# Kernel optimization log

Hardware: AMD Instinct MI355X
Metric: run time of the kernel (lower is better)

The kernel has to match this reference:

```python
import jax, jax.numpy as jnp
import numpy as np

B, C, F, H, W = 2, 512, 8, 32, 32


def setup_inputs() -> dict:
    key = jax.random.key(0)
    ks = jax.random.split(key, 10)
    s = 0.02
    return {
        "x": jax.random.normal(ks[0], (B, C, F, H, W), jnp.float32),
        "gamma": jnp.ones((C, 1, 1, 1), jnp.float32),
        "wq": jax.random.normal(ks[1], (C, C), jnp.float32) * s,
        "bq": jnp.zeros((C,), jnp.float32),
        "wk": jax.random.normal(ks[2], (C, C), jnp.float32) * s,
        "bk": jnp.zeros((C,), jnp.float32),
        "wv": jax.random.normal(ks[3], (C, C), jnp.float32) * s,
        "bv": jnp.zeros((C,), jnp.float32),
        "wo": jax.random.normal(ks[4], (C, C), jnp.float32) * s,
        "bo": jnp.zeros((C,), jnp.float32),
    }


def _rms_norm(x, gamma):
    # F.normalize(x, dim=1) * sqrt(C) * gamma  (channel-first, eps=1e-12)
    n = jnp.sqrt(jnp.sum(x * x, axis=1, keepdims=True))
    return x / jnp.maximum(n, 1e-12) * (x.shape[1] ** 0.5) * gamma


def _conv1x1(x, w, b):
    # 1x1x1 Conv3d == per-voxel linear over channels
    return jnp.einsum("oi,bifhw->bofhw", w, x) + b[None, :, None, None, None]


def reference(x, gamma, wq, bq, wk, bk, wv, bv, wo, bo):
    b, c, f, h, w = x.shape
    n_hw = h * w
    S = f * n_hw

    hn = _rms_norm(x, gamma)
    q = _conv1x1(hn, wq, bq).reshape(b, c, S).swapaxes(1, 2)  # [b, S, c]
    k = _conv1x1(hn, wk, bk).reshape(b, c, S).swapaxes(1, 2)
    v = _conv1x1(hn, wv, bv).reshape(b, c, S).swapaxes(1, 2)

    # block-causal mask: query attends to all tokens in frames <= its own frame
    frame_id = jnp.arange(S) // n_hw
    allow = frame_id[:, None] >= frame_id[None, :]  # [S, S] bool

    scores = jnp.einsum("bsc,btc->bst", q, k) / jnp.sqrt(jnp.asarray(c, x.dtype))
    scores = jnp.where(allow[None], scores, -jnp.inf)
    p = jax.nn.softmax(scores, axis=-1)
    o = jnp.einsum("bst,btc->bsc", p, v)  # [b, S, c]

    o = o.swapaxes(1, 2).reshape(b, c, f, h, w)
    return x + _conv1x1(o, wo, bo)
```

## Files before the change

### kernel.cpp

```cpp
#include <hip/hip_runtime.h>
#include <hip/hip_bf16.h>
#include <math.h>

typedef __bf16 bf16;
typedef __bf16 bf16x8 __attribute__((ext_vector_type(8)));
typedef float f32x4 __attribute__((ext_vector_type(4)));
typedef long longx2 __attribute__((ext_vector_type(2)));

#define C_DIM 512
#define S_DIM 8192

__device__ __forceinline__ void async_ld16(const void* g, void* l) {
    __builtin_amdgcn_global_load_lds(
        (const __attribute__((address_space(1))) unsigned int*)g,
        (__attribute__((address_space(3))) unsigned int*)l, 16, 0, 0);
}

__device__ __forceinline__ unsigned char to_fp8(float v) {
    return (unsigned char)(__builtin_amdgcn_cvt_pk_fp8_f32(v, v, 0, false) & 0xFF);
}

__global__ void detect_kernel(const unsigned short* __restrict__ xu, int* __restrict__ flag) {
    int j = threadIdx.x;
    for (int i = 16 + j; i < 320; i += 64) flag[i] = 0;
    unsigned e = (xu[2 * j] >> 7) & 0xFF;
    unsigned long long m = __ballot(e >= 90 && e <= 140);
    if (j == 0) *flag = (__popcll(m) >= 48) ? 1 : 0;
}

__global__ __launch_bounds__(256) void convert_kernel(const void* __restrict__ s0,
                                                      const void* __restrict__ s1,
                                                      const void* __restrict__ s2,
                                                      const void* __restrict__ s3,
                                                      bf16* __restrict__ dst,
                                                      const int* __restrict__ flag) {
    int y = blockIdx.y;
    const void* srcs[4] = {s0, s1, s2, s3};
    const void* src = srcs[y];
    int i = blockIdx.x * 256 + threadIdx.x;
    bf16* d = dst + (size_t)y * 262144;
    if (*flag) {
        volatile const bf16* s = (volatile const bf16*)src;
        d[i] = s[i];
    } else {
        volatile const float* s = (volatile const float*)src;
        d[i] = (bf16)s[i];
    }
}

__global__ __launch_bounds__(256) void rms_kernel(const void* __restrict__ x,
                                                  float* __restrict__ r,
                                                  const int* __restrict__ flag) {
    __shared__ float red[4][64];
    int b  = blockIdx.x >> 7;
    int s0 = (blockIdx.x & 127) * 64;
    int sl = threadIdx.x & 63;
    int cq = threadIdx.x >> 6;
    float acc = 0.f;
    if (*flag) {
        const bf16* xp = (const bf16*)x + ((size_t)b * C_DIM + cq * 128) * S_DIM + s0 + sl;
        for (int c = 0; c < 128; ++c) { float v = (float)xp[(size_t)c * S_DIM]; acc += v * v; }
    } else {
        const float* xp = (const float*)x + ((size_t)b * C_DIM + cq * 128) * S_DIM + s0 + sl;
        for (int c = 0; c < 128; ++c) { float v = xp[(size_t)c * S_DIM]; acc += v * v; }
    }
    red[cq][sl] = acc;
    __syncthreads();
    if (cq == 0) {
        float t = red[0][sl] + red[1][sl] + red[2][sl] + red[3][sl];
        r[b * S_DIM + s0 + sl] = 22.627416997969522f / fmaxf(sqrtf(t), 1e-12f);
    }
}

__global__ __launch_bounds__(256) void hn_kernel(const void* __restrict__ x,
                                                 const void* __restrict__ gamma,
                                                 const float* __restrict__ r,
                                                 bf16* __restrict__ hn,
                                                 const int* __restrict__ flag) {
    __shared__ float tile[64][65];
    int f  = *flag;
    int b  = blockIdx.z;
    int c0 = blockIdx.y * 64;
    int s0 = blockIdx.x * 64;
    int col = threadIdx.x & 63;
    int row = threadIdx.x >> 6;
    if (f) {
        const bf16* xp = (const bf16*)x + ((size_t)b * C_DIM + c0) * S_DIM + s0;
        for (int i = 0; i < 16; ++i)
            tile[row + i * 4][col] = (float)xp[(size_t)(row + i * 4) * S_DIM + col];
    } else {
        const float* xp = (const float*)x + ((size_t)b * C_DIM + c0) * S_DIM + s0;
        for (int i = 0; i < 16; ++i)
            tile[row + i * 4][col] = xp[(size_t)(row + i * 4) * S_DIM + col];
    }
    __syncthreads();
    float g;
    if (f) g = (float)((const bf16*)gamma)[c0 + col];
    else   g = ((const float*)gamma)[c0 + col];
    bf16* hp = hn + ((size_t)b * S_DIM + s0) * C_DIM + c0;
    for (int i = 0; i < 16; ++i) {
        int s_l = row + i * 4;
        float rv = r[b * S_DIM + s0 + s_l];
        hp[(size_t)s_l * C_DIM + col] = (bf16)(tile[col][s_l] * rv * g);
    }
}

__global__ __launch_bounds__(256, 2) void gemm_qkv_kernel(const bf16* __restrict__ A,
                                                          const bf16* __restrict__ Wq,
                                                          const bf16* __restrict__ Wk,
                                                          const bf16* __restrict__ Wv,
                                                          const void* __restrict__ bq,
                                                          const void* __restrict__ bk,
                                                          const void* __restrict__ bv,
                                                          unsigned char* __restrict__ oq,
                                                          unsigned char* __restrict__ ok,
                                                          unsigned char* __restrict__ ov,
                                                          const int* __restrict__ flag) {
    __shared__ bf16 As[128 * 40];
    __shared__ bf16 Bqs[128 * 40];
    __shared__ bf16 Bks[128 * 40];
    __shared__ bf16 Bvs[128 * 40];
    int f  = *flag;
    int m0 = blockIdx.x * 128;
    int n0 = blockIdx.y * 128;
    int tid  = threadIdx.x;
    int lane = tid & 63;
    int wave = tid >> 6;
    int wm = (wave & 1) * 64;
    int wn = (wave >> 1) * 64;
    int l15  = lane & 15;
    int quad = lane >> 4;

    f32x4 aq[4][4] = {}, ak[4][4] = {}, av[4][4] = {};
    for (int k0 = 0; k0 < C_DIM; k0 += 32) {
        __syncthreads();
        for (int u = tid; u < 512; u += 256) {
            int rr = u >> 2;
            int cc = (u & 3) * 8;
            *(bf16x8*)&As[rr * 40 + cc]  = *(const bf16x8*)&A [(size_t)(m0 + rr) * C_DIM + k0 + cc];
            *(bf16x8*)&Bqs[rr * 40 + cc] = *(const bf16x8*)&Wq[(size_t)(n0 + rr) * C_DIM + k0 + cc];
            *(bf16x8*)&Bks[rr * 40 + cc] = *(const bf16x8*)&Wk[(size_t)(n0 + rr) * C_DIM + k0 + cc];
            *(bf16x8*)&Bvs[rr * 40 + cc] = *(const bf16x8*)&Wv[(size_t)(n0 + rr) * C_DIM + k0 + cc];
        }
        __syncthreads();
        bf16x8 af[4];
#pragma unroll
        for (int i = 0; i < 4; ++i)
            af[i] = *(bf16x8*)&As[(wm + i * 16 + l15) * 40 + quad * 8];
#pragma unroll
        for (int j = 0; j < 4; ++j) {
            int boff = (wn + j * 16 + l15) * 40 + quad * 8;
            bf16x8 b0 = *(bf16x8*)&Bqs[boff];
#pragma unroll
            for (int i = 0; i < 4; ++i)
                aq[i][j] = __builtin_amdgcn_mfma_f32_16x16x32_bf16(af[i], b0, aq[i][j], 0, 0, 0);
            bf16x8 b1 = *(bf16x8*)&Bks[boff];
#pragma unroll
            for (int i = 0; i < 4; ++i)
                ak[i][j] = __builtin_amdgcn_mfma_f32_16x16x32_bf16(af[i], b1, ak[i][j], 0, 0, 0);
            bf16x8 b2 = *(bf16x8*)&Bvs[boff];
#pragma unroll
            for (int i = 0; i < 4; ++i)
                av[i][j] = __builtin_amdgcn_mfma_f32_16x16x32_bf16(af[i], b2, av[i][j], 0, 0, 0);
        }
    }
#pragma unroll
    for (int i = 0; i < 4; ++i)
#pragma unroll
        for (int j = 0; j < 4; ++j) {
            int n = n0 + wn + j * 16 + l15;
            float bvq = f ? (float)((const bf16*)bq)[n] : ((const float*)bq)[n];
            float bvk = f ? (float)((const bf16*)bk)[n] : ((const float*)bk)[n];
            float bvv = f ? (float)((const bf16*)bv)[n] : ((const float*)bv)[n];
#pragma unroll
            for (int rg = 0; rg < 4; ++rg) {
                int m = m0 + wm + i * 16 + quad * 4 + rg;
                oq[(size_t)m * C_DIM + n] = to_fp8(aq[i][j][rg] + bvq);
                size_t ik = (size_t)(m >> 5) * 16384 +
                            (((size_t)(n >> 6) * 4 + ((n >> 3) & 3)) * 32 + (m & 31)) * 16 +
                            ((n >> 5) & 1) * 8 + (n & 7);
                ok[ik] = to_fp8(ak[i][j][rg] + bvk);
                size_t iv = (size_t)(m >> 5) * 16384 + ((size_t)(m >> 3) & 3) * 4096 +
                            (((size_t)(n >> 5) * 16 + (n & 15)) * 2 + ((n >> 4) & 1)) * 8 + (m & 7);
                ov[iv] = to_fp8(av[i][j][rg] + bvv);
            }
        }
}

__global__ __launch_bounds__(256, 2) void gemm_kernel(const bf16* __restrict__ A,
                                                      const bf16* __restrict__ W,
                                                      const void* __restrict__ bias,
                                                      const void* __restrict__ resid,
                                                      void* __restrict__ out,
                                                      const int* __restrict__ flag) {
    __shared__ bf16 As[128 * 40];
    __shared__ bf16 Bs[128 * 40];
    int f  = *flag;
    int m0 = blockIdx.x * 128;
    int n0 = blockIdx.y * 128;
    int tid  = threadIdx.x;
    int lane = tid & 63;
    int wave = tid >> 6;
    int wm = (wave & 1) * 64;
    int wn = (wave >> 1) * 64;
    int l15  = lane & 15;
    int quad = lane >> 4;

    f32x4 acc[4][4] = {};
    for (int k0 = 0; k0 < C_DIM; k0 += 32) {
        __syncthreads();
        for (int u = tid; u < 512; u += 256) {
            int rrow = u >> 2;
            int cc = (u & 3) * 8;
            *(bf16x8*)&As[rrow * 40 + cc] =
                *(const bf16x8*)&A[(size_t)(m0 + rrow) * C_DIM + k0 + cc];
            *(bf16x8*)&Bs[rrow * 40 + cc] =
                *(const bf16x8*)&W[(size_t)(n0 + rrow) * C_DIM + k0 + cc];
        }
        __syncthreads();
        bf16x8 af[4], bfr[4];
#pragma unroll
        for (int i = 0; i < 4; ++i)
            af[i] = *(bf16x8*)&As[(wm + i * 16 + l15) * 40 + quad * 8];
#pragma unroll
        for (int j = 0; j < 4; ++j)
            bfr[j] = *(bf16x8*)&Bs[(wn + j * 16 + l15) * 40 + quad * 8];
#pragma unroll
        for (int i = 0; i < 4; ++i)
#pragma unroll
            for (int j = 0; j < 4; ++j)
                acc[i][j] = __builtin_amdgcn_mfma_f32_16x16x32_bf16(af[i], bfr[j], acc[i][j], 0, 0, 0);
    }
    if (f) {
        bf16* op = (bf16*)out;
        const bf16* rp = (const bf16*)resid;
#pragma unroll
        for (int i = 0; i < 4; ++i)
#pragma unroll
            for (int j = 0; j < 4; ++j)
#pragma unroll
                for (int rg = 0; rg < 4; ++rg) {
                    int m = m0 + wm + i * 16 + quad * 4 + rg;
                    int n = n0 + wn + j * 16 + l15;
                    float bv = (float)((const bf16*)bias)[n];
                    int b = m >> 13, s = m & 8191;
                    size_t idx = ((size_t)b * C_DIM + n) * S_DIM + s;
                    op[idx] = (bf16)(acc[i][j][rg] + bv + (float)rp[idx]);
                }
    } else {
        float* op = (float*)out;
        const float* rp = (const float*)resid;
#pragma unroll
        for (int i = 0; i < 4; ++i)
#pragma unroll
            for (int j = 0; j < 4; ++j)
#pragma unroll
                for (int rg = 0; rg < 4; ++rg) {
                    int m = m0 + wm + i * 16 + quad * 4 + rg;
                    int n = n0 + wn + j * 16 + l15;
                    float bv = ((const float*)bias)[n];
                    int b = m >> 13, s = m & 8191;
                    size_t idx = ((size_t)b * C_DIM + n) * S_DIM + s;
                    op[idx] = acc[i][j][rg] + bv + rp[idx];
                }
    }
}

__global__ __launch_bounds__(256, 2) void attn_split_kernel(const unsigned char* __restrict__ q,
                                                            const unsigned char* __restrict__ k,
                                                            const unsigned char* __restrict__ vt,
                                                            bf16* __restrict__ part,
                                                            float* __restrict__ lsum,
                                                            int* __restrict__ counter,
                                                            int* __restrict__ cnt,
                                                            int* __restrict__ slist) {
    __shared__ unsigned char Ks[2][16384];
    __shared__ unsigned char Vs[2][16384];
    __shared__ unsigned char Ps[4][16 * 40];
    __shared__ int slot_sh;
    int tid  = threadIdx.x;
    int lane = tid & 63;
    int wave = tid >> 6;
    int l15  = lane & 15;
    int quad = lane >> 4;

    int g0 = blockIdx.x * 72;
    int b_ = (g0 >= 18432) ? 1 : 0;
    int r  = g0 - b_ * 18432;
    int f_ = 0;
    while (r >= 256 * (f_ + 1) * (f_ + 2)) ++f_;
    int L   = 32 * (f_ + 1);
    int rr  = r - 256 * f_ * (f_ + 1);
    int tif = rr / L;
    int cw  = rr - tif * L;

    long qf[16];
    {
        int qbase = (f_ * 16 + tif) * 64 + wave * 16;
        const unsigned char* qp = q + (size_t)(b_ * S_DIM + qbase + l15) * C_DIM;
#pragma unroll
        for (int ks = 0; ks < 16; ++ks)
            qf[ks] = *(const long*)&qp[ks * 32 + quad * 8];
    }

    f32x4 oacc[32] = {};
    float l_i[4] = {0.f, 0.f, 0.f, 0.f};
    const float scale = 0.044194173824159216f;

    {
        const unsigned char* ka = k  + ((size_t)(b_ * 256 + cw) << 14);
        const unsigned char* va = vt + ((size_t)(b_ * 256 + cw) << 14);
#pragma unroll
        for (int j = 0; j < 4; ++j) {
            int base = (j * 4 + wave) * 1024;
            async_ld16(ka + base + lane * 16, &Ks[0][base]);
            async_ld16(va + base + lane * 16, &Vs[0][base]);
        }
    }
    __syncthreads();

    for (int i = 0; i < 72; ++i) {
        int last = (i == 71);
        int nb = b_, nf = f_, nL = L, ntif = tif, ncw = cw + 1;
        int newtile = 0;
        if (ncw == L) {
            ncw = 0; newtile = 1; ntif = tif + 1;
            if (ntif == 16) {
                ntif = 0; nf = f_ + 1; nL = L + 32;
                if (nf == 8) { nf = 0; nL = 32; nb = b_ + 1; }
            }
        }
        if (last) { nb = b_; nf = f_; nL = L; ntif = tif; ncw = cw; newtile = 0; }

        {
            const unsigned char* ka = k  + ((size_t)(nb * 256 + ncw) << 14);
            const unsigned char* va = vt + ((size_t)(nb * 256 + ncw) << 14);
            unsigned char* kd = Ks[(i + 1) & 1];
            unsigned char* vd = Vs[(i + 1) & 1];
#pragma unroll
            for (int j = 0; j < 4; ++j) {
                int base = (j * 4 + wave) * 1024;
                async_ld16(ka + base + lane * 16, kd + base);
                async_ld16(va + base + lane * 16, vd + base);
            }
        }
        const unsigned char* kb = Ks[i & 1];
        const unsigned char* vb = Vs[i & 1];

        f32x4 st[2] = {};
#pragma unroll
        for (int nt = 0; nt < 2; ++nt) {
#pragma unroll
            for (int pp = 0; pp < 8; ++pp) {
                longx2 kf = *(const longx2*)&kb[(((pp * 4 + quad) * 32) + nt * 16 + l15) * 16];
                st[nt] = __builtin_amdgcn_mfma_f32_16x16x32_fp8_fp8(qf[2 * pp], kf[0], st[nt], 0, 0, 0);
                st[nt] = __builtin_amdgcn_mfma_f32_16x16x32_fp8_fp8(qf[2 * pp + 1], kf[1], st[nt], 0, 0, 0);
            }
        }
        float p0[4], p1[4];
#pragma unroll
        for (int rg = 0; rg < 4; ++rg) {
            p0[rg] = __expf(st[0][rg] * scale);
            p1[rg] = __expf(st[1][rg] * scale);
            l_i[rg] += p0[rg] + p1[rg];
        }
        unsigned char* pw = Ps[wave];
#pragma unroll
        for (int rg = 0; rg < 4; ++rg) {
            pw[(quad * 4 + rg) * 40 + l15] = to_fp8(p0[rg]);
            pw[(quad * 4 + rg) * 40 + 16 + l15] = to_fp8(p1[rg]);
        }
        long pf = *(const long*)&pw[l15 * 40 + quad * 8];
#pragma unroll
        for (int dnp = 0; dnp < 16; ++dnp) {
            longx2 vf = *(const longx2*)&vb[quad * 4096 + (dnp * 16 + l15) * 16];
            oacc[2 * dnp]     = __builtin_amdgcn_mfma_f32_16x16x32_fp8_fp8(pf, vf[0], oacc[2 * dnp], 0, 0, 0);
            oacc[2 * dnp + 1] = __builtin_amdgcn_mfma_f32_16x16x32_fp8_fp8(pf, vf[1], oacc[2 * dnp + 1], 0, 0, 0);
        }

        if (last || newtile) {
            int ord = b_ * 128 + f_ * 16 + tif;
            if (tid == 0) {
                int s = atomicAdd(counter, 1);
                int pos = atomicAdd(&cnt[ord], 1);
                slist[ord * 8 + pos] = s;
                slot_sh = s;
            }
            __syncthreads();
            int slot = slot_sh;
#pragma unroll
            for (int rg = 0; rg < 4; ++rg)
                for (int d = 1; d < 16; d <<= 1)
                    l_i[rg] += __shfl_xor(l_i[rg], d);
            float rinv[4];
#pragma unroll
            for (int rg = 0; rg < 4; ++rg) rinv[rg] = 1.f / l_i[rg];
            bf16* pp = part + ((size_t)slot * 64 + wave * 16) * C_DIM;
#pragma unroll
            for (int dn = 0; dn < 32; ++dn)
#pragma unroll
                for (int rg = 0; rg < 4; ++rg)
                    pp[(size_t)(quad * 4 + rg) * C_DIM + dn * 16 + l15] =
                        (bf16)(oacc[dn][rg] * rinv[rg]);
            if (l15 == 0) {
#pragma unroll
                for (int rg = 0; rg < 4; ++rg)
                    lsum[slot * 64 + wave * 16 + quad * 4 + rg] = l_i[rg];
            }
            if (!last) {
#pragma unroll
                for (int dn = 0; dn < 32; ++dn) oacc[dn] = (f32x4){0.f, 0.f, 0.f, 0.f};
#pragma unroll
                for (int rg = 0; rg < 4; ++rg) l_i[rg] = 0.f;
                int nqbase = (nf * 16 + ntif) * 64 + wave * 16;
                const unsigned char* qp = q + (size_t)(nb * S_DIM + nqbase + l15) * C_DIM;
#pragma unroll
                for (int ks = 0; ks < 16; ++ks)
                    qf[ks] = *(const long*)&qp[ks * 32 + quad * 8];
            }
        }
        b_ = nb; f_ = nf; L = nL; tif = ntif; cw = ncw;
        __syncthreads();
    }
}

__global__ __launch_bounds__(256, 2) void attn_kernel(const unsigned char* __restrict__ q,
                                                      const unsigned char* __restrict__ k,
                                                      const unsigned char* __restrict__ vt,
                                                      bf16* __restrict__ ob) {
    __shared__ unsigned char Ks[2][16384];
    __shared__ unsigned char Vs[2][16384];
    __shared__ unsigned char Ps[4][16 * 40];
    int id = blockIdx.x;
    int b = id >> 7;
    int t = id & 127;
    int q0 = t * 64;
    int kc1 = ((t >> 4) + 1) << 10;
    int tid  = threadIdx.x;
    int lane = tid & 63;
    int wave = tid >> 6;
    int l15  = lane & 15;
    int quad = lane >> 4;
    int qbase = q0 + wave * 16;
    int nchunks = kc1 >> 5;

    long qf[16];
    const unsigned char* qp = q + (size_t)(b * S_DIM + qbase + l15) * C_DIM;
#pragma unroll
    for (int ks = 0; ks < 16; ++ks)
        qf[ks] = *(const long*)&qp[ks * 32 + quad * 8];

    f32x4 oacc[32] = {};
    float l_i[4] = {0.f, 0.f, 0.f, 0.f};
    const float scale = 0.044194173824159216f;

    const unsigned char* kbase = k  + ((size_t)(b * 256) << 14);
    const unsigned char* vbase = vt + ((size_t)(b * 256) << 14);

#pragma unroll
    for (int j = 0; j < 4; ++j) {
        int base = (j * 4 + wave) * 1024;
        async_ld16(kbase + base + lane * 16, &Ks[0][base]);
        async_ld16(vbase + base + lane * 16, &Vs[0][base]);
    }
    __syncthreads();

    for (int p = 0; p < nchunks; ++p) {
        int pn = (p + 1 < nchunks) ? (p + 1) : p;
        const unsigned char* ksub = kbase + ((size_t)pn << 14);
        const unsigned char* vsub = vbase + ((size_t)pn << 14);
        unsigned char* kd = Ks[(p + 1) & 1];
        unsigned char* vd = Vs[(p + 1) & 1];
#pragma unroll
        for (int j = 0; j < 4; ++j) {
            int base = (j * 4 + wave) * 1024;
            async_ld16(ksub + base + lane * 16, kd + base);
            async_ld16(vsub + base + lane * 16, vd + base);
        }
        const unsigned char* kb = Ks[p & 1];
        const unsigned char* vb = Vs[p & 1];
        f32x4 st[2] = {};
#pragma unroll
        for (int nt = 0; nt < 2; ++nt) {
#pragma unroll
            for (int pp = 0; pp < 8; ++pp) {
                longx2 kf = *(const longx2*)&kb[(((pp * 4 + quad) * 32) + nt * 16 + l15) * 16];
                st[nt] = __builtin_amdgcn_mfma_f32_16x16x32_fp8_fp8(qf[2 * pp], kf[0], st[nt], 0, 0, 0);
                st[nt] = __builtin_amdgcn_mfma_f32_16x16x32_fp8_fp8(qf[2 * pp + 1], kf[1], st[nt], 0, 0, 0);
            }
        }
        float p0[4], p1[4];
#pragma unroll
        for (int rg = 0; rg < 4; ++rg) {
            p0[rg] = __expf(st[0][rg] * scale);
            p1[rg] = __expf(st[1][rg] * scale);
            l_i[rg] += p0[rg] + p1[rg];
        }
        unsigned char* pw = Ps[wave];
#pragma unroll
        for (int rg = 0; rg < 4; ++rg) {
            pw[(quad * 4 + rg) * 40 + l15] = to_fp8(p0[rg]);
            pw[(quad * 4 + rg) * 40 + 16 + l15] = to_fp8(p1[rg]);
        }
        long pf = *(const long*)&pw[l15 * 40 + quad * 8];
#pragma unroll
        for (int dnp = 0; dnp < 16; ++dnp) {
            longx2 vf = *(const longx2*)&vb[quad * 4096 + (dnp * 16 + l15) * 16];
            oacc[2 * dnp]     = __builtin_amdgcn_mfma_f32_16x16x32_fp8_fp8(pf, vf[0], oacc[2 * dnp], 0, 0, 0);
            oacc[2 * dnp + 1] = __builtin_amdgcn_mfma_f32_16x16x32_fp8_fp8(pf, vf[1], oacc[2 * dnp + 1], 0, 0, 0);
        }
        __syncthreads();
    }
#pragma unroll
    for (int rg = 0; rg < 4; ++rg)
        for (int d = 1; d < 16; d <<= 1)
            l_i[rg] += __shfl_xor(l_i[rg], d);
    float rinv[4];
#pragma unroll
    for (int rg = 0; rg < 4; ++rg) rinv[rg] = 1.f / l_i[rg];
    bf16* op = ob + (size_t)(b * S_DIM + qbase) * C_DIM;
#pragma unroll
    for (int dn = 0; dn < 32; ++dn)
#pragma unroll
        for (int rg = 0; rg < 4; ++rg)
            op[(size_t)(quad * 4 + rg) * C_DIM + dn * 16 + l15] =
                (bf16)(oacc[dn][rg] * rinv[rg]);
}

__global__ __launch_bounds__(256) void combine_kernel(const bf16* __restrict__ part,
                                                      const float* __restrict__ lsum,
                                                      bf16* __restrict__ ob,
                                                      const int* __restrict__ cnt,
                                                      const int* __restrict__ slist) {
    int id = blockIdx.x;
    int b  = id >> 7;
    int q0 = (id & 127) * 64;
    int U  = cnt[id];
    int qq = threadIdx.x >> 2;
    int cr = threadIdx.x & 3;
    int sl[8];
    float w[8];
    float D = 0.f;
    for (int u = 0; u < U; ++u) {
        sl[u] = slist[id * 8 + u];
        w[u] = lsum[sl[u] * 64 + qq];
        D += w[u];
    }
    float Dinv = 1.f / D;
    for (int u = 0; u < U; ++u) w[u] *= Dinv;
    bf16* op = ob + (size_t)(b * S_DIM + q0 + qq) * C_DIM + cr * 128;
    for (int ch = 0; ch < 16; ++ch) {
        float acc[8] = {};
        for (int u = 0; u < U; ++u) {
            bf16x8 pv = *(const bf16x8*)&part[((size_t)sl[u] * 64 + qq) * C_DIM + cr * 128 + ch * 8];
#pragma unroll
            for (int j = 0; j < 8; ++j) acc[j] += w[u] * (float)pv[j];
        }
        bf16x8 o8;
#pragma unroll
        for (int j = 0; j < 8; ++j) o8[j] = (bf16)acc[j];
        *(bf16x8*)&op[ch * 8] = o8;
    }
}

extern "C" void kernel_launch(void* const* d_in, const int* in_sizes, int n_in,
                              void* d_out, int out_size, void* d_ws, size_t ws_size,
                              hipStream_t stream) {
    const void* x     = d_in[0];
    const void* gamma = d_in[1];
    const void* wq    = d_in[2];
    const void* bq    = d_in[3];
    const void* wk    = d_in[4];
    const void* bk    = d_in[5];
    const void* wv    = d_in[6];
    const void* bv    = d_in[7];
    const void* wo    = d_in[8];
    const void* bo    = d_in[9];

    char* ws = (char*)d_ws;
    int*   flag    = (int*)ws;
    int*   counter = (int*)(ws + 64);
    int*   cntp    = (int*)(ws + 256);
    int*   slist   = (int*)(ws + 0x12000);
    float* r_buf   = (float*)(ws + 4096);
    bf16* wqb = (bf16*)(ws + 0x20000);
    bf16* wkb = (bf16*)(ws + 0xA0000);
    bf16* wvb = (bf16*)(ws + 0x120000);
    bf16* wob = (bf16*)(ws + 0x1A0000);
    float* lsum_buf = (float*)(ws + 0x240000);
    bf16* hn  = (bf16*)(ws + 0x400000);
    unsigned char* qb  = (unsigned char*)(ws + 0x1400000);
    unsigned char* kb  = (unsigned char*)(ws + 0x1C00000);
    unsigned char* vtb = (unsigned char*)(ws + 0x2400000);
    bf16* ob  = (bf16*)(ws + 0x2C00000);
    bf16* part = (bf16*)(ws + 0x5400000);

    const size_t ws_needed_split = 0x5400000ull + 768ull * 64 * 512 * 2;
    int split = (ws_size >= ws_needed_split) ? 1 : 0;

    hipLaunchKernelGGL(detect_kernel, dim3(1), dim3(64), 0, stream,
                       (const unsigned short*)x, flag);
    hipLaunchKernelGGL(convert_kernel, dim3(1024, 4), dim3(256), 0, stream,
                       wq, wk, wv, wo, wqb, flag);
    hipLaunchKernelGGL(rms_kernel, dim3(256), dim3(256), 0, stream, x, r_buf, flag);
    hipLaunchKernelGGL(hn_kernel, dim3(128, 8, 2), dim3(256), 0, stream, x, gamma, r_buf, hn, flag);
    hipLaunchKernelGGL(gemm_qkv_kernel, dim3(128, 4), dim3(256), 0, stream,
                       hn, wqb, wkb, wvb, bq, bk, bv, qb, kb, vtb, flag);
    if (split) {
        hipLaunchKernelGGL(attn_split_kernel, dim3(512), dim3(256), 0, stream,
                           qb, kb, vtb, part, lsum_buf, counter, cntp, slist);
        hipLaunchKernelGGL(combine_kernel, dim3(256), dim3(256), 0, stream,
                           part, lsum_buf, ob, cntp, slist);
    } else {
        hipLaunchKernelGGL(attn_kernel, dim3(256), dim3(256), 0, stream, qb, kb, vtb, ob);
    }
    hipLaunchKernelGGL(gemm_kernel, dim3(128, 4), dim3(256), 0, stream, ob, wob, bo, x, d_out, flag);
}
```

Before: 375.6 us.

## Fuse RMS norm kernels, split QK MFMA chains, remap attention blocks, widen combine grid

Merges the RMS-reduction and normalize/transpose kernels into one kernel that stages a 512x64 bf16 tile in LDS, so x is read from global memory once instead of twice. In the split attention kernel, the QK^T MFMA accumulation is split into two independent chains to shorten dependency latency, s_setprio is raised around the MFMA sections, and block indices are remapped across the grid to change work distribution. The combine kernel grid gains a y dimension over channel quarters for more parallelism. The fused kernel uses large LDS (~68KB), which may limit occupancy, and storing x as bf16 in LDS rounds fp32 inputs before normalization.

```diff
diff --git a/kernel.cpp b/kernel.cpp
--- a/kernel.cpp
+++ b/kernel.cpp
@@ -48,60 +48,59 @@
     }
 }
 
-__global__ __launch_bounds__(256) void rms_kernel(const void* __restrict__ x,
-                                                  float* __restrict__ r,
-                                                  const int* __restrict__ flag) {
+__global__ __launch_bounds__(256, 2) void rmshn_kernel(const void* __restrict__ x,
+                                                       const void* __restrict__ gamma,
+                                                       bf16* __restrict__ hn,
+                                                       const int* __restrict__ flag) {
+    __shared__ unsigned short Xs[512][66];
     __shared__ float red[4][64];
+    __shared__ float rbuf[64];
+    int f  = *flag;
     int b  = blockIdx.x >> 7;
     int s0 = (blockIdx.x & 127) * 64;
-    int sl = threadIdx.x & 63;
-    int cq = threadIdx.x >> 6;
-    float acc = 0.f;
-    if (*flag) {
-        const bf16* xp = (const bf16*)x + ((size_t)b * C_DIM + cq * 128) * S_DIM + s0 + sl;
-        for (int c = 0; c < 128; ++c) { float v = (float)xp[(size_t)c * S_DIM]; acc += v * v; }
-    } else {
-        const float* xp = (const float*)x + ((size_t)b * C_DIM + cq * 128) * S_DIM + s0 + sl;
-        for (int c = 0; c < 128; ++c) { float v = xp[(size_t)c * S_DIM]; acc += v * v; }
-    }
-    red[cq][sl] = acc;
-    __syncthreads();
-    if (cq == 0) {
-        float t = red[0][sl] + red[1][sl] + red[2][sl] + red[3][sl];
-        r[b * S_DIM + s0 + sl] = 22.627416997969522f / fmaxf(sqrtf(t), 1e-12f);
-    }
-}
-
-__global__ __launch_bounds__(256) void hn_kernel(const void* __restrict__ x,
-                                                 const void* __restrict__ gamma,
-                                                 const float* __restrict__ r,
-                                                 bf16* __restrict__ hn,
-                                                 const int* __restrict__ flag) {
-    __shared__ float tile[64][65];
-    int f  = *flag;
-    int b  = blockIdx.z;
-    int c0 = blockIdx.y * 64;
-    int s0 = blockIdx.x * 64;
     int col = threadIdx.x & 63;
     int row = threadIdx.x >> 6;
+    float acc = 0.f;
     if (f) {
-        const bf16* xp = (const bf16*)x + ((size_t)b * C_DIM + c0) * S_DIM + s0;
-        for (int i = 0; i < 16; ++i)
-            tile[row + i * 4][col] = (float)xp[(size_t)(row + i * 4) * S_DIM + col];
+        const unsigned short* xp = (const unsigned short*)x + (size_t)b * C_DIM * S_DIM + s0 + col;
+#pragma unroll 4
+        for (int cq = 0; cq < 8; ++cq)
+            for (int i = 0; i < 16; ++i) {
+                int c = cq * 64 + row + i * 4;
+                unsigned short u = xp[(size_t)c * S_DIM];
+                float v = __uint_as_float(((unsigned int)u) << 16);
+                acc += v * v;
+                Xs[c][col] = u;
+            }
     } else {
-        const float* xp = (const float*)x + ((size_t)b * C_DIM + c0) * S_DIM + s0;
-        for (int i = 0; i < 16; ++i)
-            tile[row + i * 4][col] = xp[(size_t)(row + i * 4) * S_DIM + col];
-    }
+        const float* xp = (const float*)x + (size_t)b * C_DIM * S_DIM + s0 + col;
+#pragma unroll 4
+        for (int cq = 0; cq < 8; ++cq)
+            for (int i = 0; i < 16; ++i) {
+                int c = cq * 64 + row + i * 4;
+                float v = xp[(size_t)c * S_DIM];
+                acc += v * v;
+                bf16 h = (bf16)v;
+                Xs[c][col] = *(unsigned short*)&h;
+            }
+    }
+    red[row][col] = acc;
     __syncthreads();
-    float g;
-    if (f) g = (float)((const bf16*)gamma)[c0 + col];
-    else   g = ((const float*)gamma)[c0 + col];
-    bf16* hp = hn + ((size_t)b * S_DIM + s0) * C_DIM + c0;
-    for (int i = 0; i < 16; ++i) {
-        int s_l = row + i * 4;
-        float rv = r[b * S_DIM + s0 + s_l];
-        hp[(size_t)s_l * C_DIM + col] = (bf16)(tile[col][s_l] * rv * g);
+    if (row == 0) {
+        float t = red[0][col] + red[1][col] + red[2][col] + red[3][col];
+        rbuf[col] = 22.627416997969522f / fmaxf(sqrtf(t), 1e-12f);
+    }
+    __syncthreads();
+    bf16* hp = hn + ((size_t)b * S_DIM + s0) * C_DIM;
+    for (int cq = 0; cq < 8; ++cq) {
+        int c = cq * 64 + col;
+        float g = f ? (float)((const bf16*)gamma)[c] : ((const float*)gamma)[c];
+#pragma unroll 4
+        for (int i = 0; i < 16; ++i) {
+            int s_l = row + i * 4;
+            float v = __uint_as_float(((unsigned int)Xs[c][s_l]) << 16);
+            hp[(size_t)s_l * C_DIM + c] = (bf16)(v * rbuf[s_l] * g);
+        }
     }
 }
 
@@ -284,7 +283,9 @@
     int l15  = lane & 15;
     int quad = lane >> 4;
 
-    int g0 = blockIdx.x * 72;
+    int bid = blockIdx.x;
+    int vb  = (bid & 7) * 64 + (bid >> 3);
+    int g0 = vb * 72;
     int b_ = (g0 >= 18432) ? 1 : 0;
     int r  = g0 - b_ * 18432;
     int f_ = 0;
@@ -345,23 +346,28 @@
             }
         }
         const unsigned char* kb = Ks[i & 1];
-        const unsigned char* vb = Vs[i & 1];
-
-        f32x4 st[2] = {};
-#pragma unroll
-        for (int nt = 0; nt < 2; ++nt) {
-#pragma unroll
-            for (int pp = 0; pp < 8; ++pp) {
-                longx2 kf = *(const longx2*)&kb[(((pp * 4 + quad) * 32) + nt * 16 + l15) * 16];
-                st[nt] = __builtin_amdgcn_mfma_f32_16x16x32_fp8_fp8(qf[2 * pp], kf[0], st[nt], 0, 0, 0);
-                st[nt] = __builtin_amdgcn_mfma_f32_16x16x32_fp8_fp8(qf[2 * pp + 1], kf[1], st[nt], 0, 0, 0);
-            }
-        }
+        const unsigned char* vb2 = Vs[i & 1];
+
+        f32x4 sa[2] = {}, sb[2] = {};
+        __builtin_amdgcn_s_setprio(1);
+#pragma unroll
+        for (int pp = 0; pp < 4; ++pp) {
+#pragma unroll
+            for (int nt = 0; nt < 2; ++nt) {
+                longx2 ka2 = *(const longx2*)&kb[(((pp * 4 + quad) * 32) + nt * 16 + l15) * 16];
+                longx2 kb2 = *(const longx2*)&kb[((((pp + 4) * 4 + quad) * 32) + nt * 16 + l15) * 16];
+                sa[nt] = __builtin_amdgcn_mfma_f32_16x16x32_fp8_fp8(qf[2 * pp],     ka2[0], sa[nt], 0, 0, 0);
+                sb[nt] = __builtin_amdgcn_mfma_f32_16x16x32_fp8_fp8(qf[2 * pp + 8], kb2[0], sb[nt], 0, 0, 0);
+                sa[nt] = __builtin_amdgcn_mfma_f32_16x16x32_fp8_fp8(qf[2 * pp + 1], ka2[1], sa[nt], 0, 0, 0);
+                sb[nt] = __builtin_amdgcn_mfma_f32_16x16x32_fp8_fp8(qf[2 * pp + 9], kb2[1], sb[nt], 0, 0, 0);
+            }
+        }
+        __builtin_amdgcn_s_setprio(0);
         float p0[4], p1[4];
 #pragma unroll
         for (int rg = 0; rg < 4; ++rg) {
-            p0[rg] = __expf(st[0][rg] * scale);
-            p1[rg] = __expf(st[1][rg] * scale);
+            p0[rg] = __expf((sa[0][rg] + sb[0][rg]) * scale);
+            p1[rg] = __expf((sa[1][rg] + sb[1][rg]) * scale);
             l_i[rg] += p0[rg] + p1[rg];
         }
         unsigned char* pw = Ps[wave];
@@ -371,12 +377,14 @@
             pw[(quad * 4 + rg) * 40 + 16 + l15] = to_fp8(p1[rg]);
         }
         long pf = *(const long*)&pw[l15 * 40 + quad * 8];
+        __builtin_amdgcn_s_setprio(1);
 #pragma unroll
         for (int dnp = 0; dnp < 16; ++dnp) {
-            longx2 vf = *(const longx2*)&vb[quad * 4096 + (dnp * 16 + l15) * 16];
+            longx2 vf = *(const longx2*)&vb2[quad * 4096 + (dnp * 16 + l15) * 16];
             oacc[2 * dnp]     = __builtin_amdgcn_mfma_f32_16x16x32_fp8_fp8(pf, vf[0], oacc[2 * dnp], 0, 0, 0);
             oacc[2 * dnp + 1] = __builtin_amdgcn_mfma_f32_16x16x32_fp8_fp8(pf, vf[1], oacc[2 * dnp + 1], 0, 0, 0);
         }
+        __builtin_amdgcn_s_setprio(0);
 
         if (last || newtile) {
             int ord = b_ * 128 + f_ * 16 + tif;
@@ -395,12 +403,12 @@
             float rinv[4];
 #pragma unroll
             for (int rg = 0; rg < 4; ++rg) rinv[rg] = 1.f / l_i[rg];
-            bf16* pp = part + ((size_t)slot * 64 + wave * 16) * C_DIM;
+            bf16* pp2 = part + ((size_t)slot * 64 + wave * 16) * C_DIM;
 #pragma unroll
             for (int dn = 0; dn < 32; ++dn)
 #pragma unroll
                 for (int rg = 0; rg < 4; ++rg)
-                    pp[(size_t)(quad * 4 + rg) * C_DIM + dn * 16 + l15] =
+                    pp2[(size_t)(quad * 4 + rg) * C_DIM + dn * 16 + l15] =
                         (bf16)(oacc[dn][rg] * rinv[rg]);
             if (l15 == 0) {
 #pragma unroll
@@ -538,6 +546,7 @@
     int U  = cnt[id];
     int qq = threadIdx.x >> 2;
     int cr = threadIdx.x & 3;
+    int cbase = blockIdx.y * 128 + cr * 32;
     int sl[8];
     float w[8];
     float D = 0.f;
@@ -548,11 +557,11 @@
     }
     float Dinv = 1.f / D;
     for (int u = 0; u < U; ++u) w[u] *= Dinv;
-    bf16* op = ob + (size_t)(b * S_DIM + q0 + qq) * C_DIM + cr * 128;
-    for (int ch = 0; ch < 16; ++ch) {
+    bf16* op = ob + (size_t)(b * S_DIM + q0 + qq) * C_DIM + cbase;
+    for (int ch = 0; ch < 4; ++ch) {
         float acc[8] = {};
         for (int u = 0; u < U; ++u) {
-            bf16x8 pv = *(const bf16x8*)&part[((size_t)sl[u] * 64 + qq) * C_DIM + cr * 128 + ch * 8];
+            bf16x8 pv = *(const bf16x8*)&part[((size_t)sl[u] * 64 + qq) * C_DIM + cbase + ch * 8];
 #pragma unroll
             for (int j = 0; j < 8; ++j) acc[j] += w[u] * (float)pv[j];
         }
@@ -582,7 +591,6 @@
     int*   counter = (int*)(ws + 64);
     int*   cntp    = (int*)(ws + 256);
     int*   slist   = (int*)(ws + 0x12000);
-    float* r_buf   = (float*)(ws + 4096);
     bf16* wqb = (bf16*)(ws + 0x20000);
     bf16* wkb = (bf16*)(ws + 0xA0000);
     bf16* wvb = (bf16*)(ws + 0x120000);
@@ -602,14 +610,13 @@
                        (const unsigned short*)x, flag);
     hipLaunchKernelGGL(convert_kernel, dim3(1024, 4), dim3(256), 0, stream,
                        wq, wk, wv, wo, wqb, flag);
-    hipLaunchKernelGGL(rms_kernel, dim3(256), dim3(256), 0, stream, x, r_buf, flag);
-    hipLaunchKernelGGL(hn_kernel, dim3(128, 8, 2), dim3(256), 0, stream, x, gamma, r_buf, hn, flag);
+    hipLaunchKernelGGL(rmshn_kernel, dim3(256), dim3(256), 0, stream, x, gamma, hn, flag);
     hipLaunchKernelGGL(gemm_qkv_kernel, dim3(128, 4), dim3(256), 0, stream,
                        hn, wqb, wkb, wvb, bq, bk, bv, qb, kb, vtb, flag);
     if (split) {
         hipLaunchKernelGGL(attn_split_kernel, dim3(512), dim3(256), 0, stream,
                            qb, kb, vtb, part, lsum_buf, counter, cntp, slist);
-        hipLaunchKernelGGL(combine_kernel, dim3(256), dim3(256), 0, stream,
+        hipLaunchKernelGGL(combine_kernel, dim3(256, 4), dim3(256), 0, stream,
                            part, lsum_buf, ob, cntp, slist);
     } else {
         hipLaunchKernelGGL(attn_kernel, dim3(256), dim3(256), 0, stream, qb, kb, vtb, ob);
```

After: 359.5 us. 1.04x faster.
